# Optimization experiments

Hardware: AMD Instinct MI355X
Metric: run time of the kernel (lower is better)

The kernel has to match this reference:

```python
import jax, jax.numpy as jnp
import numpy as np

N = 100_000      # nodes
F_IN = 128       # in_channels
C = 128          # out_channels
H = 2 * C        # conv1 output dim
E = 1_000_000    # edges per graph
EPS = 1e-12      # F.normalize eps


def setup_inputs() -> dict:
    key = jax.random.key(0)
    k = jax.random.split(key, 5)
    x = jax.random.normal(k[0], (N, F_IN), jnp.float32)
    edge_index_top = jax.random.randint(k[1], (2, E), 0, N, dtype=jnp.int64)
    edge_index_last = jax.random.randint(k[2], (2, E), 0, N, dtype=jnp.int64)
    W1 = jax.random.normal(k[3], (F_IN, H), jnp.float32) / np.sqrt(F_IN)
    b1 = jnp.zeros((H,), jnp.float32)
    return {"x": x, "edge_index_top": edge_index_top,
            "edge_index_last": edge_index_last, "W1": W1, "b1": b1}


def gcn_conv(x, W, b, src, dst, n):
    """PyG GCNConv: out = D^{-1/2} (A + I) D^{-1/2} X W + b, deg over A+I."""
    xw = x @ W                                           # [N, H]
    ones = jnp.ones(src.shape[0], xw.dtype)
    deg = jax.ops.segment_sum(ones, dst, num_segments=n) + 1.0  # +1 self loop
    dinv = jax.lax.rsqrt(deg)                            # [N]
    norm = dinv[src] * dinv[dst]                         # [E]
    agg = jax.ops.segment_sum(norm[:, None] * xw[src], dst, num_segments=n)
    agg = agg + (dinv * dinv)[:, None] * xw              # self-loop term
    return agg + b


def reference(x, edge_index_top, edge_index_last, W1, b1):
    n = x.shape[0]
    # F.normalize(x, dim=1)
    xn = x / jnp.clip(jnp.linalg.norm(x, axis=1, keepdims=True), EPS)
    src_t, dst_t = edge_index_top[0], edge_index_top[1]
    ztop = gcn_conv(xn, W1, b1, src_t, dst_t, n)         # [N, H]
    # aedge = sigmoid(ztop @ ztop.T)[src, dst] without materializing NxN
    aedge = jax.nn.sigmoid(jnp.sum(ztop[src_t] * ztop[dst_t], axis=-1))  # [E]
    zlast = gcn_conv(xn, W1, b1, edge_index_last[0], edge_index_last[1], n)
    return (ztop, zlast, aedge)
```

## Files before the change

kernel.cpp:

```cpp
#include <hip/hip_runtime.h>
#include <hip/hip_bf16.h>

typedef __bf16 bf16_t;
typedef __bf16 bf16x4 __attribute__((ext_vector_type(4)));
typedef __bf16 bf16x8 __attribute__((ext_vector_type(8)));
typedef float  f32x4  __attribute__((ext_vector_type(4)));

#define N_NODES 100000
#define F_INC   128
#define HDIM    256
#define NEDGE   1000000
#define ELL_CAP 48
#define GATHER_BLKS (N_NODES / 4)
#define GEMM_BLKS   ((N_NODES / 16 + 3) / 4)
#define FILL_BLKS   ((NEDGE + 255) / 256)

__global__ void zero_cnt(int* __restrict__ cnt, int n) {
    int i = blockIdx.x * 256 + threadIdx.x;
    if (i < n) cnt[i] = 0;
}

__global__ void detect_kernel(const int* __restrict__ eit, const int* __restrict__ eil,
                              int* __restrict__ flags) {
    int lane = threadIdx.x & 63;
    const int* p = (threadIdx.x < 64) ? eit : eil;
    int s = (p[2 * lane + 1] != 0) ? 1 : 0;
    #pragma unroll
    for (int off = 1; off < 64; off <<= 1) s += __shfl_xor(s, off, 64);
    if (lane == 0) flags[(threadIdx.x < 64) ? 0 : 1] = (s == 0) ? 1 : 0;
}

__global__ void wprep_kernel(const float* __restrict__ W1, bf16_t* __restrict__ wlay,
                             bf16_t* __restrict__ xw, bf16_t* __restrict__ zb) {
    int t = blockIdx.x * 256 + threadIdx.x;
    if (blockIdx.x == 0) {
        xw[(size_t)N_NODES * HDIM + threadIdx.x] = (bf16_t)0.f;
        zb[(size_t)N_NODES * HDIM + threadIdx.x] = (bf16_t)0.f;
    }
    int j = t & 7, lane = (t >> 3) & 63, kk = (t >> 9) & 3, nt = t >> 11;
    int m = lane & 15, q = lane >> 4;
    int k = kk * 32 + q * 8 + j;
    int n = nt * 16 + m;
    wlay[t] = (bf16_t)W1[k * HDIM + n];
}

__device__ __forceinline__ void gemm_body(int w, int lane, const float* __restrict__ x,
                                          const bf16_t* __restrict__ wlay,
                                          bf16_t* __restrict__ xw) {
    if (w >= N_NODES / 16) return;
    int m = lane & 15, q = lane >> 4;
    int r0 = w * 16;
    int row = r0 + m;
    const float4* xr = (const float4*)(x + (size_t)row * F_INC);
    float4 u[8];
    #pragma unroll
    for (int kk = 0; kk < 4; kk++) {
        u[2 * kk]     = xr[kk * 8 + q * 2];
        u[2 * kk + 1] = xr[kk * 8 + q * 2 + 1];
    }
    float ss = 0.f;
    #pragma unroll
    for (int j = 0; j < 8; j++)
        ss += u[j].x * u[j].x + u[j].y * u[j].y + u[j].z * u[j].z + u[j].w * u[j].w;
    ss += __shfl_xor(ss, 16, 64);
    ss += __shfl_xor(ss, 32, 64);
    float rv = 1.0f / fmaxf(sqrtf(ss), 1e-12f);
    bf16x8 a[4];
    #pragma unroll
    for (int kk = 0; kk < 4; kk++) {
        float4 p0 = u[2 * kk], p1 = u[2 * kk + 1];
        a[kk][0] = (bf16_t)(p0.x * rv); a[kk][1] = (bf16_t)(p0.y * rv);
        a[kk][2] = (bf16_t)(p0.z * rv); a[kk][3] = (bf16_t)(p0.w * rv);
        a[kk][4] = (bf16_t)(p1.x * rv); a[kk][5] = (bf16_t)(p1.y * rv);
        a[kk][6] = (bf16_t)(p1.z * rv); a[kk][7] = (bf16_t)(p1.w * rv);
    }
    const bf16x8* wl = (const bf16x8*)wlay;
    #pragma unroll
    for (int nt = 0; nt < 16; nt++) {
        f32x4 c = {0.f, 0.f, 0.f, 0.f};
        c = __builtin_amdgcn_mfma_f32_16x16x32_bf16(a[0], wl[(nt * 4 + 0) * 64 + lane], c, 0, 0, 0);
        c = __builtin_amdgcn_mfma_f32_16x16x32_bf16(a[1], wl[(nt * 4 + 1) * 64 + lane], c, 0, 0, 0);
        c = __builtin_amdgcn_mfma_f32_16x16x32_bf16(a[2], wl[(nt * 4 + 2) * 64 + lane], c, 0, 0, 0);
        c = __builtin_amdgcn_mfma_f32_16x16x32_bf16(a[3], wl[(nt * 4 + 3) * 64 + lane], c, 0, 0, 0);
        #pragma unroll
        for (int i = 0; i < 4; i++) {
            xw[(size_t)(r0 + q * 4 + i) * HDIM + nt * 16 + m] = (bf16_t)c[i];
        }
    }
}

__device__ __forceinline__ void fill2_body(int e, const int* __restrict__ ei,
                                           const int* __restrict__ flag,
                                           int* __restrict__ cnt, int* __restrict__ ell2) {
    if (e >= NEDGE) return;
    int f = *flag;
    int src = ei[e << f];
    int dst = ei[(NEDGE + e) << f];
    int slot = atomicAdd(&cnt[dst], 1);
    if (slot < ELL_CAP) {
        int2 pr; pr.x = src; pr.y = e;
        ((int2*)ell2)[(size_t)dst * ELL_CAP + slot] = pr;
    }
}

__device__ __forceinline__ void fill_body(int e, const int* __restrict__ ei,
                                          const int* __restrict__ flag,
                                          int* __restrict__ cnt, int* __restrict__ ell) {
    if (e >= NEDGE) return;
    int f = *flag;
    int src = ei[e << f];
    int dst = ei[(NEDGE + e) << f];
    int slot = atomicAdd(&cnt[dst], 1);
    if (slot < ELL_CAP) ell[dst * ELL_CAP + slot] = src;
}

__global__ __launch_bounds__(256) void gemm_fill_kernel(const float* __restrict__ x,
                                                        const bf16_t* __restrict__ wlay,
                                                        bf16_t* __restrict__ xw,
                                                        const int* __restrict__ ei,
                                                        const int* __restrict__ flag,
                                                        int* __restrict__ cnt,
                                                        int* __restrict__ ell2) {
    if (blockIdx.x < GEMM_BLKS) {
        gemm_body(blockIdx.x * 4 + (threadIdx.x >> 6), threadIdx.x & 63, x, wlay, xw);
    } else {
        fill2_body((blockIdx.x - GEMM_BLKS) * 256 + threadIdx.x, ei, flag, cnt, ell2);
    }
}

__global__ void dinvpad_kernel(const int* __restrict__ cnt, float* __restrict__ dinv,
                               int* __restrict__ ell, int paired) {
    int i = blockIdx.x * 256 + threadIdx.x;
    if (i >= N_NODES) {
        if (i == N_NODES) dinv[N_NODES] = 0.f;
        return;
    }
    int c = cnt[i];
    dinv[i] = rsqrtf((float)c + 1.0f);
    int deg = (c > ELL_CAP) ? ELL_CAP : c;
    int r4 = (deg + 3) & ~3;
    if (paired) {
        int2 pr; pr.x = N_NODES; pr.y = -1;
        for (int s = deg; s < r4; s++) ((int2*)ell)[(size_t)i * ELL_CAP + s] = pr;
    } else {
        for (int s = deg; s < r4; s++) ell[i * ELL_CAP + s] = N_NODES;
    }
}

template<bool PAIRED>
__device__ __forceinline__ void gather_body(int i, int lane, const int* __restrict__ ell,
                                            const int* __restrict__ cnt,
                                            const float* __restrict__ dinv,
                                            const bf16_t* __restrict__ xw,
                                            const float* __restrict__ b1,
                                            float* __restrict__ out,
                                            bf16_t* __restrict__ zb) {
    float di = dinv[i];
    const bf16x4* xws = (const bf16x4*)xw;
    bf16x4 sv = xws[(size_t)i * 64 + lane];
    float acc0 = di * (float)sv.x;
    float acc1 = di * (float)sv.y;
    float acc2 = di * (float)sv.z;
    float acc3 = di * (float)sv.w;
    int deg = cnt[i];
    if (deg > ELL_CAP) deg = ELL_CAP;
    int nit = (deg + 3) >> 2;
    int4 sa, sb;
    if (PAIRED) {
        const int4* e8 = (const int4*)ell + (size_t)i * (ELL_CAP / 2);
        sa = e8[0]; sb = e8[1];
        for (int b = 0; b < nit; b++) {
            int bn = (b + 1 < nit) ? (b + 1) : b;
            int4 na = e8[2 * bn], nb = e8[2 * bn + 1];
            int s0 = sa.x, s1 = sa.z, s2 = sb.x, s3 = sb.z;
            float d0 = dinv[s0], d1 = dinv[s1], d2 = dinv[s2], d3 = dinv[s3];
            bf16x4 v0 = xws[(size_t)s0 * 64 + lane];
            bf16x4 v1 = xws[(size_t)s1 * 64 + lane];
            bf16x4 v2 = xws[(size_t)s2 * 64 + lane];
            bf16x4 v3 = xws[(size_t)s3 * 64 + lane];
            acc0 += d0 * (float)v0.x + d1 * (float)v1.x + d2 * (float)v2.x + d3 * (float)v3.x;
            acc1 += d0 * (float)v0.y + d1 * (float)v1.y + d2 * (float)v2.y + d3 * (float)v3.y;
            acc2 += d0 * (float)v0.z + d1 * (float)v1.z + d2 * (float)v2.z + d3 * (float)v3.z;
            acc3 += d0 * (float)v0.w + d1 * (float)v1.w + d2 * (float)v2.w + d3 * (float)v3.w;
            sa = na; sb = nb;
        }
    } else {
        const int4* el4 = (const int4*)(ell + (size_t)i * ELL_CAP);
        sa = el4[0];
        for (int b = 0; b < nit; b++) {
            int bn = (b + 1 < nit) ? (b + 1) : b;
            int4 na = el4[bn];
            int s0 = sa.x, s1 = sa.y, s2 = sa.z, s3 = sa.w;
            float d0 = dinv[s0], d1 = dinv[s1], d2 = dinv[s2], d3 = dinv[s3];
            bf16x4 v0 = xws[(size_t)s0 * 64 + lane];
            bf16x4 v1 = xws[(size_t)s1 * 64 + lane];
            bf16x4 v2 = xws[(size_t)s2 * 64 + lane];
            bf16x4 v3 = xws[(size_t)s3 * 64 + lane];
            acc0 += d0 * (float)v0.x + d1 * (float)v1.x + d2 * (float)v2.x + d3 * (float)v3.x;
            acc1 += d0 * (float)v0.y + d1 * (float)v1.y + d2 * (float)v2.y + d3 * (float)v3.y;
            acc2 += d0 * (float)v0.z + d1 * (float)v1.z + d2 * (float)v2.z + d3 * (float)v3.z;
            acc3 += d0 * (float)v0.w + d1 * (float)v1.w + d2 * (float)v2.w + d3 * (float)v3.w;
            sa = na;
        }
    }
    float4 bv = ((const float4*)b1)[lane];
    f32x4 o;
    o[0] = di * acc0 + bv.x;
    o[1] = di * acc1 + bv.y;
    o[2] = di * acc2 + bv.z;
    o[3] = di * acc3 + bv.w;
    __builtin_nontemporal_store(o, (f32x4*)out + (size_t)i * 64 + lane);
    if (zb) {
        bf16x4 zo;
        zo.x = (bf16_t)o[0]; zo.y = (bf16_t)o[1]; zo.z = (bf16_t)o[2]; zo.w = (bf16_t)o[3];
        ((bf16x4*)zb)[(size_t)i * 64 + lane] = zo;
    }
}

__global__ __launch_bounds__(256) void gather_fill_kernel(const int* __restrict__ ell2,
                                                          const int* __restrict__ cnt,
                                                          const float* __restrict__ dinv,
                                                          const bf16_t* __restrict__ xw,
                                                          const float* __restrict__ b1,
                                                          float* __restrict__ out,
                                                          bf16_t* __restrict__ zb,
                                                          const int* __restrict__ ei_l,
                                                          const int* __restrict__ flag_l,
                                                          int* __restrict__ cnt_l,
                                                          int* __restrict__ ell_l) {
    if (blockIdx.x < FILL_BLKS) {
        fill_body(blockIdx.x * 256 + threadIdx.x, ei_l, flag_l, cnt_l, ell_l);
    } else {
        gather_body<true>((blockIdx.x - FILL_BLKS) * 4 + (threadIdx.x >> 6), threadIdx.x & 63,
                          ell2, cnt, dinv, xw, b1, out, zb);
    }
}

__device__ __forceinline__ void aedge_dst_body(int i, int lane, const int* __restrict__ ell2,
                                               const int* __restrict__ cnt,
                                               const bf16_t* __restrict__ zb,
                                               float* __restrict__ aedge) {
    int sub = lane & 15, g = lane >> 4;
    const bf16x8* z8 = (const bf16x8*)zb;
    bf16x8 d0 = z8[(size_t)i * 32 + sub * 2];
    bf16x8 d1 = z8[(size_t)i * 32 + sub * 2 + 1];
    int deg = cnt[i];
    if (deg > ELL_CAP) deg = ELL_CAP;
    int nit = (deg + 3) >> 2;
    if (nit == 0) return;
    const int2* pr = (const int2*)ell2 + (size_t)i * ELL_CAP;
    int2 pe = pr[g];
    for (int b = 0; b < nit; b++) {
        int bn = (b + 1 < nit) ? (b + 1) : b;
        int2 pn = pr[bn * 4 + g];
        int src = pe.x, eid = pe.y;
        bf16x8 a0 = z8[(size_t)src * 32 + sub * 2];
        bf16x8 a1 = z8[(size_t)src * 32 + sub * 2 + 1];
        float p = 0.f;
        #pragma unroll
        for (int j = 0; j < 8; j++)
            p += (float)a0[j] * (float)d0[j] + (float)a1[j] * (float)d1[j];
        #pragma unroll
        for (int off = 1; off < 16; off <<= 1) p += __shfl_xor(p, off, 64);
        if (sub == 0 && eid >= 0)
            __builtin_nontemporal_store(1.0f / (1.0f + __expf(-p)), &aedge[eid]);
        pe = pn;
    }
}

__global__ __launch_bounds__(256) void fused_last_kernel(const int* __restrict__ ell_l,
                                                         const int* __restrict__ cnt_l,
                                                         const float* __restrict__ dinv_l,
                                                         const bf16_t* __restrict__ xw,
                                                         const float* __restrict__ b1,
                                                         float* __restrict__ out1,
                                                         const int* __restrict__ ell2_t,
                                                         const int* __restrict__ cnt_t,
                                                         const bf16_t* __restrict__ zb,
                                                         float* __restrict__ aedge) {
    int lane = threadIdx.x & 63;
    int node = (blockIdx.x >> 1) * 4 + (threadIdx.x >> 6);
    if (blockIdx.x & 1) {
        aedge_dst_body(node, lane, ell2_t, cnt_t, zb, aedge);
    } else {
        gather_body<false>(node, lane, ell_l, cnt_l, dinv_l, xw, b1, out1, (bf16_t*)0);
    }
}

extern "C" void kernel_launch(void* const* d_in, const int* in_sizes, int n_in,
                              void* d_out, int out_size, void* d_ws, size_t ws_size,
                              hipStream_t stream) {
    const float* x       = (const float*)d_in[0];
    const int*   ei_top  = (const int*)d_in[1];
    const int*   ei_last = (const int*)d_in[2];
    const float* W1      = (const float*)d_in[3];
    const float* b1      = (const float*)d_in[4];
    float* out = (float*)d_out;

    char* ws = (char*)d_ws;
    bf16_t* xw     = (bf16_t*)(ws);
    bf16_t* zb     = (bf16_t*)(ws + 51201024);
    int*    ell2t  = (int*)  (ws + 102402048);
    int*    ell_l  = (int*)  (ws + 140802048);
    float*  dinv_t = (float*)(ws + 160002048);
    float*  dinv_l = (float*)(ws + 160402112);
    int*    cnt_t  = (int*)  (ws + 160802176);
    int*    cnt_l  = (int*)  (ws + 161202176);
    bf16_t* wlay   = (bf16_t*)(ws + 161602176);
    int*    flags  = (int*)  (ws + 161667712);

    zero_cnt<<<(2 * N_NODES + 255) / 256, 256, 0, stream>>>(cnt_t, 2 * N_NODES);
    detect_kernel<<<1, 128, 0, stream>>>(ei_top, ei_last, flags);
    wprep_kernel<<<128, 256, 0, stream>>>(W1, wlay, xw, zb);
    gemm_fill_kernel<<<GEMM_BLKS + FILL_BLKS, 256, 0, stream>>>(x, wlay, xw,
                                                                ei_top, flags, cnt_t, ell2t);
    dinvpad_kernel<<<(N_NODES + 256) / 256 + 1, 256, 0, stream>>>(cnt_t, dinv_t, ell2t, 1);
    gather_fill_kernel<<<FILL_BLKS + GATHER_BLKS, 256, 0, stream>>>(
        ell2t, cnt_t, dinv_t, xw, b1, out, zb, ei_last, flags + 1, cnt_l, ell_l);
    dinvpad_kernel<<<(N_NODES + 256) / 256 + 1, 256, 0, stream>>>(cnt_l, dinv_l, ell_l, 0);
    fused_last_kernel<<<2 * GATHER_BLKS, 256, 0, stream>>>(
        ell_l, cnt_l, dinv_l, xw, b1, out + (size_t)N_NODES * HDIM,
        ell2t, cnt_t, zb, out + (size_t)2 * N_NODES * HDIM);
}
```

Before: 637.9 us.

## Fuse both graph gathers per node and restructure fills and aedge pass

Both edge-list fills now run in the GEMM kernel, and a single padding kernel handles both graphs. One gather kernel aggregates the top and last graphs for each node, so each node's own xw row is read once and both gathers are interleaved. The aedge pass becomes its own kernel that handles two edges per iteration and uses nontemporal index loads, with the top ELL padded to multiples of 8. This reduces the number of launches and shares loads between the graphs. In exchange, the dual loop runs to the larger of the two degrees and does dummy loads for the shorter list, and the aedge work no longer overlaps with a gather.

```diff
diff --git a/kernel.cpp b/kernel.cpp
--- a/kernel.cpp
+++ b/kernel.cpp
@@ -5,6 +5,8 @@
 typedef __bf16 bf16x4 __attribute__((ext_vector_type(4)));
 typedef __bf16 bf16x8 __attribute__((ext_vector_type(8)));
 typedef float  f32x4  __attribute__((ext_vector_type(4)));
+typedef int    i32x2  __attribute__((ext_vector_type(2)));
+typedef int    i32x4  __attribute__((ext_vector_type(4)));
 
 #define N_NODES 100000
 #define F_INC   128
@@ -117,173 +119,152 @@
 __global__ __launch_bounds__(256) void gemm_fill_kernel(const float* __restrict__ x,
                                                         const bf16_t* __restrict__ wlay,
                                                         bf16_t* __restrict__ xw,
-                                                        const int* __restrict__ ei,
-                                                        const int* __restrict__ flag,
-                                                        int* __restrict__ cnt,
-                                                        int* __restrict__ ell2) {
+                                                        const int* __restrict__ ei_t,
+                                                        const int* __restrict__ flags,
+                                                        int* __restrict__ cnt_t,
+                                                        int* __restrict__ ell2t,
+                                                        const int* __restrict__ ei_l,
+                                                        int* __restrict__ cnt_l,
+                                                        int* __restrict__ ell_l) {
     if (blockIdx.x < GEMM_BLKS) {
         gemm_body(blockIdx.x * 4 + (threadIdx.x >> 6), threadIdx.x & 63, x, wlay, xw);
+    } else if (blockIdx.x < GEMM_BLKS + FILL_BLKS) {
+        fill2_body((blockIdx.x - GEMM_BLKS) * 256 + threadIdx.x, ei_t, flags, cnt_t, ell2t);
     } else {
-        fill2_body((blockIdx.x - GEMM_BLKS) * 256 + threadIdx.x, ei, flag, cnt, ell2);
-    }
-}
-
-__global__ void dinvpad_kernel(const int* __restrict__ cnt, float* __restrict__ dinv,
-                               int* __restrict__ ell, int paired) {
+        fill_body((blockIdx.x - GEMM_BLKS - FILL_BLKS) * 256 + threadIdx.x, ei_l, flags + 1,
+                  cnt_l, ell_l);
+    }
+}
+
+__global__ void dinvpad_both(const int* __restrict__ cnt_t, const int* __restrict__ cnt_l,
+                             float* __restrict__ dinv_t, float* __restrict__ dinv_l,
+                             int* __restrict__ ell2t, int* __restrict__ ell_l) {
     int i = blockIdx.x * 256 + threadIdx.x;
     if (i >= N_NODES) {
-        if (i == N_NODES) dinv[N_NODES] = 0.f;
+        if (i == N_NODES) { dinv_t[N_NODES] = 0.f; dinv_l[N_NODES] = 0.f; }
         return;
     }
-    int c = cnt[i];
-    dinv[i] = rsqrtf((float)c + 1.0f);
-    int deg = (c > ELL_CAP) ? ELL_CAP : c;
-    int r4 = (deg + 3) & ~3;
-    if (paired) {
-        int2 pr; pr.x = N_NODES; pr.y = -1;
-        for (int s = deg; s < r4; s++) ((int2*)ell)[(size_t)i * ELL_CAP + s] = pr;
-    } else {
-        for (int s = deg; s < r4; s++) ell[i * ELL_CAP + s] = N_NODES;
-    }
-}
-
-template<bool PAIRED>
-__device__ __forceinline__ void gather_body(int i, int lane, const int* __restrict__ ell,
-                                            const int* __restrict__ cnt,
-                                            const float* __restrict__ dinv,
-                                            const bf16_t* __restrict__ xw,
-                                            const float* __restrict__ b1,
-                                            float* __restrict__ out,
-                                            bf16_t* __restrict__ zb) {
-    float di = dinv[i];
+    int ct = cnt_t[i];
+    dinv_t[i] = rsqrtf((float)ct + 1.0f);
+    int dt = (ct > ELL_CAP) ? ELL_CAP : ct;
+    int r8 = (dt + 7) & ~7;
+    int2 pr; pr.x = N_NODES; pr.y = -1;
+    for (int s = dt; s < r8; s++) ((int2*)ell2t)[(size_t)i * ELL_CAP + s] = pr;
+    int cl = cnt_l[i];
+    dinv_l[i] = rsqrtf((float)cl + 1.0f);
+    int dl = (cl > ELL_CAP) ? ELL_CAP : cl;
+    int r4 = (dl + 3) & ~3;
+    for (int s = dl; s < r4; s++) ell_l[(size_t)i * ELL_CAP + s] = N_NODES;
+}
+
+__global__ __launch_bounds__(256) void dual_gather_kernel(const int* __restrict__ ell2t,
+                                                          const int* __restrict__ cnt_t,
+                                                          const float* __restrict__ dinv_t,
+                                                          const int* __restrict__ ell_l,
+                                                          const int* __restrict__ cnt_l,
+                                                          const float* __restrict__ dinv_l,
+                                                          const bf16_t* __restrict__ xw,
+                                                          const float* __restrict__ b1,
+                                                          float* __restrict__ out0,
+                                                          float* __restrict__ out1,
+                                                          bf16_t* __restrict__ zb) {
+    int i = blockIdx.x * 4 + (threadIdx.x >> 6);
+    int lane = threadIdx.x & 63;
     const bf16x4* xws = (const bf16x4*)xw;
     bf16x4 sv = xws[(size_t)i * 64 + lane];
-    float acc0 = di * (float)sv.x;
-    float acc1 = di * (float)sv.y;
-    float acc2 = di * (float)sv.z;
-    float acc3 = di * (float)sv.w;
-    int deg = cnt[i];
-    if (deg > ELL_CAP) deg = ELL_CAP;
-    int nit = (deg + 3) >> 2;
-    int4 sa, sb;
-    if (PAIRED) {
-        const int4* e8 = (const int4*)ell + (size_t)i * (ELL_CAP / 2);
-        sa = e8[0]; sb = e8[1];
-        for (int b = 0; b < nit; b++) {
-            int bn = (b + 1 < nit) ? (b + 1) : b;
-            int4 na = e8[2 * bn], nb = e8[2 * bn + 1];
-            int s0 = sa.x, s1 = sa.z, s2 = sb.x, s3 = sb.z;
-            float d0 = dinv[s0], d1 = dinv[s1], d2 = dinv[s2], d3 = dinv[s3];
-            bf16x4 v0 = xws[(size_t)s0 * 64 + lane];
-            bf16x4 v1 = xws[(size_t)s1 * 64 + lane];
-            bf16x4 v2 = xws[(size_t)s2 * 64 + lane];
-            bf16x4 v3 = xws[(size_t)s3 * 64 + lane];
-            acc0 += d0 * (float)v0.x + d1 * (float)v1.x + d2 * (float)v2.x + d3 * (float)v3.x;
-            acc1 += d0 * (float)v0.y + d1 * (float)v1.y + d2 * (float)v2.y + d3 * (float)v3.y;
-            acc2 += d0 * (float)v0.z + d1 * (float)v1.z + d2 * (float)v2.z + d3 * (float)v3.z;
-            acc3 += d0 * (float)v0.w + d1 * (float)v1.w + d2 * (float)v2.w + d3 * (float)v3.w;
-            sa = na; sb = nb;
-        }
-    } else {
-        const int4* el4 = (const int4*)(ell + (size_t)i * ELL_CAP);
-        sa = el4[0];
-        for (int b = 0; b < nit; b++) {
-            int bn = (b + 1 < nit) ? (b + 1) : b;
-            int4 na = el4[bn];
-            int s0 = sa.x, s1 = sa.y, s2 = sa.z, s3 = sa.w;
-            float d0 = dinv[s0], d1 = dinv[s1], d2 = dinv[s2], d3 = dinv[s3];
-            bf16x4 v0 = xws[(size_t)s0 * 64 + lane];
-            bf16x4 v1 = xws[(size_t)s1 * 64 + lane];
-            bf16x4 v2 = xws[(size_t)s2 * 64 + lane];
-            bf16x4 v3 = xws[(size_t)s3 * 64 + lane];
-            acc0 += d0 * (float)v0.x + d1 * (float)v1.x + d2 * (float)v2.x + d3 * (float)v3.x;
-            acc1 += d0 * (float)v0.y + d1 * (float)v1.y + d2 * (float)v2.y + d3 * (float)v3.y;
-            acc2 += d0 * (float)v0.z + d1 * (float)v1.z + d2 * (float)v2.z + d3 * (float)v3.z;
-            acc3 += d0 * (float)v0.w + d1 * (float)v1.w + d2 * (float)v2.w + d3 * (float)v3.w;
-            sa = na;
-        }
+    float dt = dinv_t[i], dl = dinv_l[i];
+    float at0 = dt * (float)sv.x, at1 = dt * (float)sv.y;
+    float at2 = dt * (float)sv.z, at3 = dt * (float)sv.w;
+    float al0 = dl * (float)sv.x, al1 = dl * (float)sv.y;
+    float al2 = dl * (float)sv.z, al3 = dl * (float)sv.w;
+    int degt = cnt_t[i]; if (degt > ELL_CAP) degt = ELL_CAP;
+    int degl = cnt_l[i]; if (degl > ELL_CAP) degl = ELL_CAP;
+    int nt4 = (degt + 3) >> 2, nl4 = (degl + 3) >> 2;
+    int nit = nt4 > nl4 ? nt4 : nl4;
+    const i32x4* e8  = (const i32x4*)ell2t + (size_t)i * (ELL_CAP / 2);
+    const i32x4* el4 = (const i32x4*)(ell_l + (size_t)i * ELL_CAP);
+    for (int b = 0; b < nit; b++) {
+        bool ht = b < nt4, hl = b < nl4;
+        int bt = ht ? 2 * b : 0;
+        int bl = hl ? b : 0;
+        i32x4 ta = __builtin_nontemporal_load(e8 + bt);
+        i32x4 tb = __builtin_nontemporal_load(e8 + bt + 1);
+        i32x4 la = __builtin_nontemporal_load(el4 + bl);
+        int t0 = ht ? ta[0] : N_NODES, t1 = ht ? ta[2] : N_NODES;
+        int t2 = ht ? tb[0] : N_NODES, t3 = ht ? tb[2] : N_NODES;
+        int l0 = hl ? la[0] : N_NODES, l1 = hl ? la[1] : N_NODES;
+        int l2 = hl ? la[2] : N_NODES, l3 = hl ? la[3] : N_NODES;
+        bf16x4 vt0 = xws[(size_t)t0 * 64 + lane];
+        bf16x4 vt1 = xws[(size_t)t1 * 64 + lane];
+        bf16x4 vt2 = xws[(size_t)t2 * 64 + lane];
+        bf16x4 vt3 = xws[(size_t)t3 * 64 + lane];
+        bf16x4 vl0 = xws[(size_t)l0 * 64 + lane];
+        bf16x4 vl1 = xws[(size_t)l1 * 64 + lane];
+        bf16x4 vl2 = xws[(size_t)l2 * 64 + lane];
+        bf16x4 vl3 = xws[(size_t)l3 * 64 + lane];
+        float w0 = dinv_t[t0], w1 = dinv_t[t1], w2 = dinv_t[t2], w3 = dinv_t[t3];
+        float u0 = dinv_l[l0], u1 = dinv_l[l1], u2 = dinv_l[l2], u3 = dinv_l[l3];
+        at0 += w0 * (float)vt0.x + w1 * (float)vt1.x + w2 * (float)vt2.x + w3 * (float)vt3.x;
+        at1 += w0 * (float)vt0.y + w1 * (float)vt1.y + w2 * (float)vt2.y + w3 * (float)vt3.y;
+        at2 += w0 * (float)vt0.z + w1 * (float)vt1.z + w2 * (float)vt2.z + w3 * (float)vt3.z;
+        at3 += w0 * (float)vt0.w + w1 * (float)vt1.w + w2 * (float)vt2.w + w3 * (float)vt3.w;
+        al0 += u0 * (float)vl0.x + u1 * (float)vl1.x + u2 * (float)vl2.x + u3 * (float)vl3.x;
+        al1 += u0 * (float)vl0.y + u1 * (float)vl1.y + u2 * (float)vl2.y + u3 * (float)vl3.y;
+        al2 += u0 * (float)vl0.z + u1 * (float)vl1.z + u2 * (float)vl2.z + u3 * (float)vl3.z;
+        al3 += u0 * (float)vl0.w + u1 * (float)vl1.w + u2 * (float)vl2.w + u3 * (float)vl3.w;
     }
     float4 bv = ((const float4*)b1)[lane];
-    f32x4 o;
-    o[0] = di * acc0 + bv.x;
-    o[1] = di * acc1 + bv.y;
-    o[2] = di * acc2 + bv.z;
-    o[3] = di * acc3 + bv.w;
-    __builtin_nontemporal_store(o, (f32x4*)out + (size_t)i * 64 + lane);
-    if (zb) {
-        bf16x4 zo;
-        zo.x = (bf16_t)o[0]; zo.y = (bf16_t)o[1]; zo.z = (bf16_t)o[2]; zo.w = (bf16_t)o[3];
-        ((bf16x4*)zb)[(size_t)i * 64 + lane] = zo;
-    }
-}
-
-__global__ __launch_bounds__(256) void gather_fill_kernel(const int* __restrict__ ell2,
-                                                          const int* __restrict__ cnt,
-                                                          const float* __restrict__ dinv,
-                                                          const bf16_t* __restrict__ xw,
-                                                          const float* __restrict__ b1,
-                                                          float* __restrict__ out,
-                                                          bf16_t* __restrict__ zb,
-                                                          const int* __restrict__ ei_l,
-                                                          const int* __restrict__ flag_l,
-                                                          int* __restrict__ cnt_l,
-                                                          int* __restrict__ ell_l) {
-    if (blockIdx.x < FILL_BLKS) {
-        fill_body(blockIdx.x * 256 + threadIdx.x, ei_l, flag_l, cnt_l, ell_l);
-    } else {
-        gather_body<true>((blockIdx.x - FILL_BLKS) * 4 + (threadIdx.x >> 6), threadIdx.x & 63,
-                          ell2, cnt, dinv, xw, b1, out, zb);
-    }
-}
-
-__device__ __forceinline__ void aedge_dst_body(int i, int lane, const int* __restrict__ ell2,
-                                               const int* __restrict__ cnt,
-                                               const bf16_t* __restrict__ zb,
-                                               float* __restrict__ aedge) {
+    f32x4 o0, o1;
+    o0[0] = dt * at0 + bv.x; o0[1] = dt * at1 + bv.y;
+    o0[2] = dt * at2 + bv.z; o0[3] = dt * at3 + bv.w;
+    o1[0] = dl * al0 + bv.x; o1[1] = dl * al1 + bv.y;
+    o1[2] = dl * al2 + bv.z; o1[3] = dl * al3 + bv.w;
+    __builtin_nontemporal_store(o0, (f32x4*)out0 + (size_t)i * 64 + lane);
+    __builtin_nontemporal_store(o1, (f32x4*)out1 + (size_t)i * 64 + lane);
+    bf16x4 zo;
+    zo.x = (bf16_t)o0[0]; zo.y = (bf16_t)o0[1]; zo.z = (bf16_t)o0[2]; zo.w = (bf16_t)o0[3];
+    ((bf16x4*)zb)[(size_t)i * 64 + lane] = zo;
+}
+
+__global__ __launch_bounds__(256) void aedge_kernel(const int* __restrict__ ell2,
+                                                    const int* __restrict__ cnt,
+                                                    const bf16_t* __restrict__ zb,
+                                                    float* __restrict__ aedge) {
+    int i = blockIdx.x * 4 + (threadIdx.x >> 6);
+    int lane = threadIdx.x & 63;
     int sub = lane & 15, g = lane >> 4;
     const bf16x8* z8 = (const bf16x8*)zb;
     bf16x8 d0 = z8[(size_t)i * 32 + sub * 2];
     bf16x8 d1 = z8[(size_t)i * 32 + sub * 2 + 1];
     int deg = cnt[i];
     if (deg > ELL_CAP) deg = ELL_CAP;
-    int nit = (deg + 3) >> 2;
-    if (nit == 0) return;
-    const int2* pr = (const int2*)ell2 + (size_t)i * ELL_CAP;
-    int2 pe = pr[g];
+    int nit = (deg + 7) >> 3;
+    const i32x2* pr = (const i32x2*)ell2 + (size_t)i * ELL_CAP;
     for (int b = 0; b < nit; b++) {
-        int bn = (b + 1 < nit) ? (b + 1) : b;
-        int2 pn = pr[bn * 4 + g];
-        int src = pe.x, eid = pe.y;
-        bf16x8 a0 = z8[(size_t)src * 32 + sub * 2];
-        bf16x8 a1 = z8[(size_t)src * 32 + sub * 2 + 1];
-        float p = 0.f;
+        i32x2 pA = __builtin_nontemporal_load(pr + b * 8 + g);
+        i32x2 pB = __builtin_nontemporal_load(pr + b * 8 + 4 + g);
+        int sA = pA[0], sB = pB[0];
+        bf16x8 a0 = z8[(size_t)sA * 32 + sub * 2];
+        bf16x8 a1 = z8[(size_t)sA * 32 + sub * 2 + 1];
+        bf16x8 c0 = z8[(size_t)sB * 32 + sub * 2];
+        bf16x8 c1 = z8[(size_t)sB * 32 + sub * 2 + 1];
+        float p = 0.f, q = 0.f;
         #pragma unroll
-        for (int j = 0; j < 8; j++)
+        for (int j = 0; j < 8; j++) {
             p += (float)a0[j] * (float)d0[j] + (float)a1[j] * (float)d1[j];
+            q += (float)c0[j] * (float)d0[j] + (float)c1[j] * (float)d1[j];
+        }
         #pragma unroll
-        for (int off = 1; off < 16; off <<= 1) p += __shfl_xor(p, off, 64);
-        if (sub == 0 && eid >= 0)
-            __builtin_nontemporal_store(1.0f / (1.0f + __expf(-p)), &aedge[eid]);
-        pe = pn;
-    }
-}
-
-__global__ __launch_bounds__(256) void fused_last_kernel(const int* __restrict__ ell_l,
-                                                         const int* __restrict__ cnt_l,
-                                                         const float* __restrict__ dinv_l,
-                                                         const bf16_t* __restrict__ xw,
-                                                         const float* __restrict__ b1,
-                                                         float* __restrict__ out1,
-                                                         const int* __restrict__ ell2_t,
-                                                         const int* __restrict__ cnt_t,
-                                                         const bf16_t* __restrict__ zb,
-                                                         float* __restrict__ aedge) {
-    int lane = threadIdx.x & 63;
-    int node = (blockIdx.x >> 1) * 4 + (threadIdx.x >> 6);
-    if (blockIdx.x & 1) {
-        aedge_dst_body(node, lane, ell2_t, cnt_t, zb, aedge);
-    } else {
-        gather_body<false>(node, lane, ell_l, cnt_l, dinv_l, xw, b1, out1, (bf16_t*)0);
+        for (int off = 1; off < 16; off <<= 1) {
+            p += __shfl_xor(p, off, 64);
+            q += __shfl_xor(q, off, 64);
+        }
+        if (sub == 0) {
+            if (pA[1] >= 0)
+                __builtin_nontemporal_store(1.0f / (1.0f + __expf(-p)), &aedge[pA[1]]);
+            if (pB[1] >= 0)
+                __builtin_nontemporal_store(1.0f / (1.0f + __expf(-q)), &aedge[pB[1]]);
+        }
     }
 }
 
@@ -312,13 +293,13 @@
     zero_cnt<<<(2 * N_NODES + 255) / 256, 256, 0, stream>>>(cnt_t, 2 * N_NODES);
     detect_kernel<<<1, 128, 0, stream>>>(ei_top, ei_last, flags);
     wprep_kernel<<<128, 256, 0, stream>>>(W1, wlay, xw, zb);
-    gemm_fill_kernel<<<GEMM_BLKS + FILL_BLKS, 256, 0, stream>>>(x, wlay, xw,
-                                                                ei_top, flags, cnt_t, ell2t);
-    dinvpad_kernel<<<(N_NODES + 256) / 256 + 1, 256, 0, stream>>>(cnt_t, dinv_t, ell2t, 1);
-    gather_fill_kernel<<<FILL_BLKS + GATHER_BLKS, 256, 0, stream>>>(
-        ell2t, cnt_t, dinv_t, xw, b1, out, zb, ei_last, flags + 1, cnt_l, ell_l);
-    dinvpad_kernel<<<(N_NODES + 256) / 256 + 1, 256, 0, stream>>>(cnt_l, dinv_l, ell_l, 0);
-    fused_last_kernel<<<2 * GATHER_BLKS, 256, 0, stream>>>(
-        ell_l, cnt_l, dinv_l, xw, b1, out + (size_t)N_NODES * HDIM,
-        ell2t, cnt_t, zb, out + (size_t)2 * N_NODES * HDIM);
-}
+    gemm_fill_kernel<<<GEMM_BLKS + 2 * FILL_BLKS, 256, 0, stream>>>(
+        x, wlay, xw, ei_top, flags, cnt_t, ell2t, ei_last, cnt_l, ell_l);
+    dinvpad_both<<<(N_NODES + 256) / 256 + 1, 256, 0, stream>>>(cnt_t, cnt_l,
+                                                                dinv_t, dinv_l, ell2t, ell_l);
+    dual_gather_kernel<<<GATHER_BLKS, 256, 0, stream>>>(
+        ell2t, cnt_t, dinv_t, ell_l, cnt_l, dinv_l, xw, b1,
+        out, out + (size_t)N_NODES * HDIM, zb);
+    aedge_kernel<<<GATHER_BLKS, 256, 0, stream>>>(ell2t, cnt_t, zb,
+                                                  out + (size_t)2 * N_NODES * HDIM);
+}
```

After: 708.7 us. +11.1%, slower.
